# Optimization experiments

Hardware: AMD Instinct MI355X
Metric: run time of the kernel (lower is better)

The kernel has to match this reference:

```python
import jax, jax.numpy as jnp
import numpy as np

RGB2GRAY = jnp.array([0.299, 0.587, 0.114], dtype=jnp.float32)

H_IMG, W_IMG = 1080, 1920
NUM, GRID_Y, GRID_X, GRID_W = 1, 16, 16, 8


def _identity_grids(num, grid_y, grid_x, grid_w):
    ident = jnp.array([1., 0, 0, 0, 0, 1., 0, 0, 0, 0, 1., 0], dtype=jnp.float32)
    return jnp.broadcast_to(ident, (num, grid_y, grid_x, grid_w, 12))


def setup_inputs() -> dict:
    key = jax.random.key(0)
    k1, k2 = jax.random.split(key)
    rgb = jax.random.uniform(k1, (3, H_IMG, W_IMG), dtype=jnp.float32)
    # learned grids = identity affine + small perturbation (so slicing is non-trivial)
    grids = _identity_grids(NUM, GRID_Y, GRID_X, GRID_W) \
        + 0.05 * jax.random.normal(k2, (NUM, GRID_Y, GRID_X, GRID_W, 12), dtype=jnp.float32)
    return {"rgb": rgb, "grids": grids, "idx": 0}


def _bilateral_slice(grid, guidance):
    """Trilinear slice. grid: (Hg, Wg, L, 12); guidance: (Hi, Wi) in [0,1].
    Returns (Hi, Wi, 12)."""
    Hg, Wg, L, _ = grid.shape
    Hi, Wi = guidance.shape
    # align_corners-style pixel -> grid coords
    gy = jnp.linspace(0.0, Hg - 1.0, Hi, dtype=jnp.float32)[:, None]   # (Hi,1)
    gx = jnp.linspace(0.0, Wg - 1.0, Wi, dtype=jnp.float32)[None, :]   # (1,Wi)
    gz = jnp.clip(guidance, 0.0, 1.0) * (L - 1.0)                      # (Hi,Wi)

    fy = jnp.floor(gy); wy = gy - fy
    fx = jnp.floor(gx); wx = gx - fx
    fz = jnp.floor(gz); wz = gz - fz
    y0 = jnp.clip(fy.astype(jnp.int32), 0, Hg - 1); y1 = jnp.clip(y0 + 1, 0, Hg - 1)
    x0 = jnp.clip(fx.astype(jnp.int32), 0, Wg - 1); x1 = jnp.clip(x0 + 1, 0, Wg - 1)
    z0 = jnp.clip(fz.astype(jnp.int32), 0, L - 1);  z1 = jnp.clip(z0 + 1, 0, L - 1)

    out = jnp.zeros((Hi, Wi, 12), dtype=grid.dtype)
    for yi, wyi in ((y0, 1.0 - wy), (y1, wy)):
        for xi, wxi in ((x0, 1.0 - wx), (x1, wx)):
            for zi, wzi in ((z0, 1.0 - wz), (z1, wz)):
                w = (wyi * wxi * wzi)[..., None]          # (Hi,Wi,1)
                out = out + grid[yi, xi, zi] * w          # gather -> (Hi,Wi,12)
    return out


def reference(rgb, grids, idx):
    grid = grids[idx]                         # (Hg, Wg, L, 12)
    rgb_hwc = jnp.transpose(rgb, (1, 2, 0))   # (H, W, 3)
    gray = jnp.tensordot(rgb_hwc, RGB2GRAY, axes=([-1], [0]))  # (H, W)
    affine = _bilateral_slice(grid, gray)     # (H, W, 12)
    affine_mat = affine.reshape(-1, 3, 4)     # (H*W, 3, 4)
    rgb_flat = rgb_hwc.reshape(-1, 3)         # (H*W, 3)
    res_rgb = jnp.einsum('nij,nj->ni', affine_mat[..., :3], rgb_flat) + affine_mat[..., 3]
    return (affine_mat, res_rgb)
```

## Files before the change

### kernel.cpp

```cpp
#include <hip/hip_runtime.h>

#define H_IMG 1080
#define W_IMG 1920
#define HW_PIX (H_IMG * W_IMG)
#define GRID_Y 16
#define GRID_X 16
#define GRID_L 8
#define CELL_F 12

__global__ __launch_bounds__(256) void bilateral_grid_kernel(
    const float* __restrict__ rgb,
    const float* __restrict__ grids,
    const int* __restrict__ idxp,
    float* __restrict__ out)
{
    int p = blockIdx.x * blockDim.x + threadIdx.x;
    if (p >= HW_PIX) return;

    int y = p / W_IMG;
    int x = p - y * W_IMG;

    const float* grid = grids + (size_t)idxp[0] * (GRID_Y * GRID_X * GRID_L * CELL_F);

    float r = rgb[p];
    float g = rgb[HW_PIX + p];
    float b = rgb[2 * HW_PIX + p];

    float gray = 0.299f * r + 0.587f * g + 0.114f * b;

    float gy = (float)y * (15.0f / 1079.0f);
    float gx = (float)x * (15.0f / 1919.0f);
    float gz = fminf(fmaxf(gray, 0.0f), 1.0f) * 7.0f;

    float fy = floorf(gy), wy = gy - fy;
    float fx = floorf(gx), wx = gx - fx;
    float fz = floorf(gz), wz = gz - fz;

    int y0 = min(max((int)fy, 0), GRID_Y - 1); int y1 = min(y0 + 1, GRID_Y - 1);
    int x0 = min(max((int)fx, 0), GRID_X - 1); int x1 = min(x0 + 1, GRID_X - 1);
    int z0 = min(max((int)fz, 0), GRID_L - 1); int z1 = min(z0 + 1, GRID_L - 1);

    int   ys[2] = {y0, y1};  float wys[2] = {1.0f - wy, wy};
    int   xs[2] = {x0, x1};  float wxs[2] = {1.0f - wx, wx};
    int   zs[2] = {z0, z1};  float wzs[2] = {1.0f - wz, wz};

    float4 acc0 = make_float4(0.f, 0.f, 0.f, 0.f);
    float4 acc1 = make_float4(0.f, 0.f, 0.f, 0.f);
    float4 acc2 = make_float4(0.f, 0.f, 0.f, 0.f);

#pragma unroll
    for (int a = 0; a < 2; ++a) {
#pragma unroll
        for (int c = 0; c < 2; ++c) {
#pragma unroll
            for (int d = 0; d < 2; ++d) {
                float w = wys[a] * wxs[c] * wzs[d];
                const float4* cell = (const float4*)(grid +
                    (size_t)((ys[a] * GRID_X + xs[c]) * GRID_L + zs[d]) * CELL_F);
                float4 c0 = cell[0];
                float4 c1 = cell[1];
                float4 c2 = cell[2];
                acc0.x = fmaf(w, c0.x, acc0.x);
                acc0.y = fmaf(w, c0.y, acc0.y);
                acc0.z = fmaf(w, c0.z, acc0.z);
                acc0.w = fmaf(w, c0.w, acc0.w);
                acc1.x = fmaf(w, c1.x, acc1.x);
                acc1.y = fmaf(w, c1.y, acc1.y);
                acc1.z = fmaf(w, c1.z, acc1.z);
                acc1.w = fmaf(w, c1.w, acc1.w);
                acc2.x = fmaf(w, c2.x, acc2.x);
                acc2.y = fmaf(w, c2.y, acc2.y);
                acc2.z = fmaf(w, c2.z, acc2.z);
                acc2.w = fmaf(w, c2.w, acc2.w);
            }
        }
    }

    float4* ao = (float4*)out + (size_t)p * 3;
    ao[0] = acc0;
    ao[1] = acc1;
    ao[2] = acc2;

    float res0 = fmaf(acc0.x, r, fmaf(acc0.y, g, fmaf(acc0.z, b, acc0.w)));
    float res1 = fmaf(acc1.x, r, fmaf(acc1.y, g, fmaf(acc1.z, b, acc1.w)));
    float res2 = fmaf(acc2.x, r, fmaf(acc2.y, g, fmaf(acc2.z, b, acc2.w)));

    float* ro = out + (size_t)HW_PIX * 12 + (size_t)p * 3;
    ro[0] = res0;
    ro[1] = res1;
    ro[2] = res2;
}

extern "C" void kernel_launch(void* const* d_in, const int* in_sizes, int n_in,
                              void* d_out, int out_size, void* d_ws, size_t ws_size,
                              hipStream_t stream) {
    const float* rgb   = (const float*)d_in[0];
    const float* grids = (const float*)d_in[1];
    const int*   idx   = (const int*)d_in[2];
    float*       out   = (float*)d_out;

    int threads = 256;
    int blocks = (HW_PIX + threads - 1) / threads;
    bilateral_grid_kernel<<<blocks, threads, 0, stream>>>(rgb, grids, idx, out);
}
```

Before: 171.4 us.

## Pre-interpolate grid along y into shared memory per row segment

Each block now handles a 192-pixel segment of one row, launched on a 2D grid. At block start it loads the grid cells the segment needs and blends them along y into a 96-float4 shared-memory slab. Each thread then does a 4-tap bilinear lookup in x and z from shared memory instead of 8 gathered global cell reads. This cuts the gather traffic and the FMAs per pixel, at the cost of a __syncthreads and a smaller block size. The kernel remains dominated by the output writes, about 60 bytes per pixel.

```diff
diff --git a/kernel.cpp b/kernel.cpp
--- a/kernel.cpp
+++ b/kernel.cpp
@@ -3,24 +3,55 @@
 #define H_IMG 1080
 #define W_IMG 1920
 #define HW_PIX (H_IMG * W_IMG)
-#define GRID_Y 16
-#define GRID_X 16
-#define GRID_L 8
-#define CELL_F 12
+#define GY 16
+#define GX 16
+#define GL 8
+#define CF 12
+#define SEG 192
 
-__global__ __launch_bounds__(256) void bilateral_grid_kernel(
+__global__ __launch_bounds__(192) void bg_kernel(
     const float* __restrict__ rgb,
     const float* __restrict__ grids,
     const int* __restrict__ idxp,
     float* __restrict__ out)
 {
-    int p = blockIdx.x * blockDim.x + threadIdx.x;
-    if (p >= HW_PIX) return;
+    __shared__ float4 sg[96];
 
-    int y = p / W_IMG;
-    int x = p - y * W_IMG;
+    const int tid = threadIdx.x;
+    const int y = blockIdx.y;
+    const int xbase = blockIdx.x * SEG;
 
-    const float* grid = grids + (size_t)idxp[0] * (GRID_Y * GRID_X * GRID_L * CELL_F);
+    const float* grid = grids + (size_t)idxp[0] * (GY * GX * GL * CF);
+
+    float gyv = (float)y * (15.0f / 1079.0f);
+    float fy = floorf(gyv);
+    float wy = gyv - fy;
+    int y0 = min(max((int)fy, 0), GY - 1);
+    int y1 = min(y0 + 1, GY - 1);
+
+    int xc0 = (int)floorf((float)xbase * (15.0f / 1919.0f));
+
+    if (tid < 96) {
+        int xi  = tid / 24;
+        int rem = tid - xi * 24;
+        int z   = rem / 3;
+        int c4  = rem - z * 3;
+        int xc  = min(xc0 + xi, GX - 1);
+        const float4* c0 = (const float4*)(grid + (size_t)((y0 * GX + xc) * GL + z) * CF) + c4;
+        const float4* c1 = (const float4*)(grid + (size_t)((y1 * GX + xc) * GL + z) * CF) + c4;
+        float4 a = *c0, b = *c1;
+        float wy0 = 1.0f - wy;
+        float4 r;
+        r.x = wy0 * a.x + wy * b.x;
+        r.y = wy0 * a.y + wy * b.y;
+        r.z = wy0 * a.z + wy * b.z;
+        r.w = wy0 * a.w + wy * b.w;
+        sg[tid] = r;
+    }
+    __syncthreads();
+
+    const int x = xbase + tid;
+    const int p = y * W_IMG + x;
 
     float r = rgb[p];
     float g = rgb[HW_PIX + p];
@@ -28,62 +59,48 @@
 
     float gray = 0.299f * r + 0.587f * g + 0.114f * b;
 
-    float gy = (float)y * (15.0f / 1079.0f);
-    float gx = (float)x * (15.0f / 1919.0f);
+    float gxv = (float)x * (15.0f / 1919.0f);
+    float fx = floorf(gxv), wx = gxv - fx;
     float gz = fminf(fmaxf(gray, 0.0f), 1.0f) * 7.0f;
-
-    float fy = floorf(gy), wy = gy - fy;
-    float fx = floorf(gx), wx = gx - fx;
     float fz = floorf(gz), wz = gz - fz;
 
-    int y0 = min(max((int)fy, 0), GRID_Y - 1); int y1 = min(y0 + 1, GRID_Y - 1);
-    int x0 = min(max((int)fx, 0), GRID_X - 1); int x1 = min(x0 + 1, GRID_X - 1);
-    int z0 = min(max((int)fz, 0), GRID_L - 1); int z1 = min(z0 + 1, GRID_L - 1);
+    int x0g = min(max((int)fx, 0), GX - 1);
+    int x1g = min(x0g + 1, GX - 1);
+    int xi0 = x0g - xc0;
+    int xi1 = x1g - xc0;
+    int z0 = min(max((int)fz, 0), GL - 1);
+    int z1 = min(z0 + 1, GL - 1);
 
-    int   ys[2] = {y0, y1};  float wys[2] = {1.0f - wy, wy};
-    int   xs[2] = {x0, x1};  float wxs[2] = {1.0f - wx, wx};
-    int   zs[2] = {z0, z1};  float wzs[2] = {1.0f - wz, wz};
+    float w00 = (1.0f - wx) * (1.0f - wz);
+    float w01 = (1.0f - wx) * wz;
+    float w10 = wx * (1.0f - wz);
+    float w11 = wx * wz;
 
-    float4 acc0 = make_float4(0.f, 0.f, 0.f, 0.f);
-    float4 acc1 = make_float4(0.f, 0.f, 0.f, 0.f);
-    float4 acc2 = make_float4(0.f, 0.f, 0.f, 0.f);
+    const float4* A = sg + (xi0 * 24 + z0 * 3);
+    const float4* B = sg + (xi0 * 24 + z1 * 3);
+    const float4* C = sg + (xi1 * 24 + z0 * 3);
+    const float4* D = sg + (xi1 * 24 + z1 * 3);
 
+    float4 acc[3];
 #pragma unroll
-    for (int a = 0; a < 2; ++a) {
-#pragma unroll
-        for (int c = 0; c < 2; ++c) {
-#pragma unroll
-            for (int d = 0; d < 2; ++d) {
-                float w = wys[a] * wxs[c] * wzs[d];
-                const float4* cell = (const float4*)(grid +
-                    (size_t)((ys[a] * GRID_X + xs[c]) * GRID_L + zs[d]) * CELL_F);
-                float4 c0 = cell[0];
-                float4 c1 = cell[1];
-                float4 c2 = cell[2];
-                acc0.x = fmaf(w, c0.x, acc0.x);
-                acc0.y = fmaf(w, c0.y, acc0.y);
-                acc0.z = fmaf(w, c0.z, acc0.z);
-                acc0.w = fmaf(w, c0.w, acc0.w);
-                acc1.x = fmaf(w, c1.x, acc1.x);
-                acc1.y = fmaf(w, c1.y, acc1.y);
-                acc1.z = fmaf(w, c1.z, acc1.z);
-                acc1.w = fmaf(w, c1.w, acc1.w);
-                acc2.x = fmaf(w, c2.x, acc2.x);
-                acc2.y = fmaf(w, c2.y, acc2.y);
-                acc2.z = fmaf(w, c2.z, acc2.z);
-                acc2.w = fmaf(w, c2.w, acc2.w);
-            }
-        }
+    for (int j = 0; j < 3; ++j) {
+        float4 va = A[j], vb = B[j], vc = C[j], vd = D[j];
+        float4 o;
+        o.x = fmaf(w00, va.x, fmaf(w01, vb.x, fmaf(w10, vc.x, w11 * vd.x)));
+        o.y = fmaf(w00, va.y, fmaf(w01, vb.y, fmaf(w10, vc.y, w11 * vd.y)));
+        o.z = fmaf(w00, va.z, fmaf(w01, vb.z, fmaf(w10, vc.z, w11 * vd.z)));
+        o.w = fmaf(w00, va.w, fmaf(w01, vb.w, fmaf(w10, vc.w, w11 * vd.w)));
+        acc[j] = o;
     }
 
     float4* ao = (float4*)out + (size_t)p * 3;
-    ao[0] = acc0;
-    ao[1] = acc1;
-    ao[2] = acc2;
+    ao[0] = acc[0];
+    ao[1] = acc[1];
+    ao[2] = acc[2];
 
-    float res0 = fmaf(acc0.x, r, fmaf(acc0.y, g, fmaf(acc0.z, b, acc0.w)));
-    float res1 = fmaf(acc1.x, r, fmaf(acc1.y, g, fmaf(acc1.z, b, acc1.w)));
-    float res2 = fmaf(acc2.x, r, fmaf(acc2.y, g, fmaf(acc2.z, b, acc2.w)));
+    float res0 = fmaf(acc[0].x, r, fmaf(acc[0].y, g, fmaf(acc[0].z, b, acc[0].w)));
+    float res1 = fmaf(acc[1].x, r, fmaf(acc[1].y, g, fmaf(acc[1].z, b, acc[1].w)));
+    float res2 = fmaf(acc[2].x, r, fmaf(acc[2].y, g, fmaf(acc[2].z, b, acc[2].w)));
 
     float* ro = out + (size_t)HW_PIX * 12 + (size_t)p * 3;
     ro[0] = res0;
@@ -99,7 +116,7 @@
     const int*   idx   = (const int*)d_in[2];
     float*       out   = (float*)d_out;
 
-    int threads = 256;
-    int blocks = (HW_PIX + threads - 1) / threads;
-    bilateral_grid_kernel<<<blocks, threads, 0, stream>>>(rgb, grids, idx, out);
+    dim3 grid(W_IMG / SEG, H_IMG);
+    dim3 block(SEG);
+    bg_kernel<<<grid, block, 0, stream>>>(rgb, grids, idx, out);
 }
```

New measurement: 154.0 us. -10.1%, faster.
